# Kernel tuning notes

Measured on AMD Instinct MI355X. Metric: run time of the kernel, lower is better.

## Reference

```python
import jax, jax.numpy as jnp
import numpy as np

H, C = 16, 5           # GAT heads, per-head out channels
SIZE = 500             # max_pool_x size (time bins)
GAT_SLOPE, ACT_SLOPE = 0.2, 0.01


def _lrelu(x, s):
    return jnp.where(x >= 0, x, s * x)


def _gat(x, src, dst, ea, mask, W, We, a_s, a_d, a_e, b):
    # PyG GATConv: shared src/dst lin, edge_dim, self-loops already appended by caller
    N = x.shape[0]
    xp = (x @ W.T).reshape(N, H, C)                                   # [N,H,C]
    al = (jnp.einsum('nhc,hc->nh', xp, a_s)[src]
          + jnp.einsum('nhc,hc->nh', xp, a_d)[dst]
          + jnp.einsum('ehc,hc->eh', (ea @ We.T).reshape(-1, H, C), a_e))  # [E,H]
    al = _lrelu(al, GAT_SLOPE)
    if mask is not None:  # masked-out edges contribute nothing (equivalent to edge removal)
        al = jnp.where(mask[:, None], al, -jnp.inf)
    m = jax.ops.segment_max(al, dst, num_segments=N)                  # finite: every node has a self-loop
    e = jnp.exp(al - m[dst])
    coef = e / jax.ops.segment_sum(e, dst, num_segments=N)[dst]       # segment softmax over incoming edges
    out = jax.ops.segment_sum(coef[:, :, None] * xp[src], dst, num_segments=N)
    return out.reshape(N, H * C) + b


def _conv(x, w, b):
    y = jax.lax.conv_general_dilated(x, w, (2,), [(1, 1)],
                                     dimension_numbers=('NCH', 'OIH', 'NCH'))
    return y + b[None, :, None]


def _mlp(z, w1, b1, w2, b2, w3, b3):
    z = _lrelu(z @ w1.T + b1, ACT_SLOPE)
    z = _lrelu(z @ w2.T + b2, ACT_SLOPE)
    return z @ w3.T + b3


def _forward(x, edge_attr,
             gat1_W, gat1_We, gat1_as, gat1_ad, gat1_ae, gat1_b,
             gat2_W, gat2_We, gat2_as, gat2_ad, gat2_ae, gat2_b,
             conv1_w, conv1_b, conv2_w, conv2_b, conv3_w, conv3_b,
             chi_w1, chi_b1, chi_w2, chi_b2, chi_w3, chi_b3,
             rp_w1, rp_b1, rp_w2, rp_b2, rp_w3, rp_b3,
             t0_w1, t0_b1, t0_w2, t0_b2, t0_w3, t0_b3,
             edge_index, num_graphs):
    N = x.shape[0]
    loops = jnp.arange(N, dtype=edge_index.dtype)
    src = jnp.concatenate([edge_index[0], loops])
    dst = jnp.concatenate([edge_index[1], loops])
    ea = jnp.concatenate([edge_attr, jnp.zeros((N, edge_attr.shape[1]), edge_attr.dtype)], axis=0)
    timing = x[:, 2].astype(jnp.int32)   # non-differentiable, like .to(torch.long)

    h = _gat(x, src, dst, ea, None, gat1_W, gat1_We, gat1_as, gat1_ad, gat1_ae, gat1_b)
    mask2 = jnp.concatenate([edge_attr[:, 0] > 1.0, jnp.ones((N,), bool)])  # EdgeV[:,0]>1 + self loops
    h = _gat(h, src, dst, ea, mask2, gat2_W, gat2_We, gat2_as, gat2_ad, gat2_ae, gat2_b)

    # max_pool_x(cluster=Timing, batch, size=500): scatter-max into B*500 slots,
    # empty slots -> 0 (torch_scatter semantics); then view(-1, 80, 500)
    pooled = jax.ops.segment_max(h, timing, num_segments=num_graphs * SIZE)
    pooled = jnp.where(jnp.isfinite(pooled), pooled, 0.0)
    z = pooled.reshape(num_graphs, H * C, SIZE)

    z = _lrelu(_conv(z, conv1_w, conv1_b), ACT_SLOPE)   # [B,16,247]
    z = _lrelu(_conv(z, conv2_w, conv2_b), ACT_SLOPE)   # [B,16,120]
    z = _lrelu(_conv(z, conv3_w, conv3_b), ACT_SLOPE)   # [B,16,57]
    L = z.shape[-1]
    nw = (L - 10) // 10 + 1                              # MaxPool1d(k=10,s=10) -> 5
    z = z[..., :nw * 10].reshape(z.shape[0], z.shape[1], nw, 10).max(-1)
    z = z.reshape(z.shape[0], -1)                        # [B,80]

    chi0 = jnp.tanh(_mlp(z, chi_w1, chi_b1, chi_w2, chi_b2, chi_w3, chi_b3))
    rp = _mlp(z, rp_w1, rp_b1, rp_w2, rp_b2, rp_w3, rp_b3)
    t0 = _mlp(z, t0_w1, t0_b1, t0_w2, t0_b2, t0_w3, t0_b3)
    return jnp.concatenate([chi0, rp, t0], axis=1)       # [B,3]


def setup_inputs() -> dict:
    key = jax.random.key(0)
    ki = iter(jax.random.split(key, 50))
    N, E, B = 100_000, 1_200_000, 64
    x = jax.random.normal(next(ki), (N, 5), jnp.float32)
    timing = jax.random.randint(next(ki), (N,), 0, SIZE)
    x = x.at[:, 2].set(timing.astype(jnp.float32))       # Timing column holds integer bins
    src = jax.random.randint(next(ki), (E,), 0, N, dtype=jnp.int32)
    off = jax.random.randint(next(ki), (E,), 1, N, dtype=jnp.int32)
    dst = (src + off) % N                                # no pre-existing self-loops (PyG strips them)
    edge_index = jnp.stack([src, dst])
    edge_attr = jax.random.uniform(next(ki), (E, 2), jnp.float32) * 3.0  # ~2/3 pass col0>1 mask
    batch = jnp.sort(jax.random.randint(next(ki), (N,), 0, B, dtype=jnp.int32))

    def p(shape, scale=0.1):
        return jax.random.normal(next(ki), shape, jnp.float32) * scale

    return dict(
        x=x, edge_attr=edge_attr,
        gat1_W=p((80, 5)), gat1_We=p((80, 2)), gat1_as=p((16, 5)), gat1_ad=p((16, 5)), gat1_ae=p((16, 5)), gat1_b=p((80,)),
        gat2_W=p((80, 80)), gat2_We=p((80, 2)), gat2_as=p((16, 5)), gat2_ad=p((16, 5)), gat2_ae=p((16, 5)), gat2_b=p((80,)),
        conv1_w=p((16, 80, 10)), conv1_b=p((16,)),
        conv2_w=p((16, 16, 10)), conv2_b=p((16,)),
        conv3_w=p((16, 16, 10)), conv3_b=p((16,)),
        chi_w1=p((128, 80)), chi_b1=p((128,)), chi_w2=p((128, 128)), chi_b2=p((128,)), chi_w3=p((1, 128)), chi_b3=p((1,)),
        rp_w1=p((128, 80)), rp_b1=p((128,)), rp_w2=p((128, 128)), rp_b2=p((128,)), rp_w3=p((1, 128)), rp_b3=p((1,)),
        t0_w1=p((128, 80)), t0_b1=p((128,)), t0_w2=p((128, 128)), t0_b2=p((128,)), t0_w3=p((1, 128)), t0_b3=p((1,)),
        edge_index=edge_index, batch=batch, num_graphs=B)


def reference(x, edge_attr,
              gat1_W, gat1_We, gat1_as, gat1_ad, gat1_ae, gat1_b,
              gat2_W, gat2_We, gat2_as, gat2_ad, gat2_ae, gat2_b,
              conv1_w, conv1_b, conv2_w, conv2_b, conv3_w, conv3_b,
              chi_w1, chi_b1, chi_w2, chi_b2, chi_w3, chi_b3,
              rp_w1, rp_b1, rp_w2, rp_b2, rp_w3, rp_b3,
              t0_w1, t0_b1, t0_w2, t0_b2, t0_w3, t0_b3,
              edge_index, batch, num_graphs):
    del batch  # only used in torch to compute batch_size (passed here as num_graphs)
    return _forward(x, edge_attr,
                    gat1_W, gat1_We, gat1_as, gat1_ad, gat1_ae, gat1_b,
                    gat2_W, gat2_We, gat2_as, gat2_ad, gat2_ae, gat2_b,
                    conv1_w, conv1_b, conv2_w, conv2_b, conv3_w, conv3_b,
                    chi_w1, chi_b1, chi_w2, chi_b2, chi_w3, chi_b3,
                    rp_w1, rp_b1, rp_w2, rp_b2, rp_w3, rp_b3,
                    t0_w1, t0_b1, t0_w2, t0_b2, t0_w3, t0_b3,
                    edge_index, num_graphs)
```

## Files before the change

### kernel.cpp

```cpp
#include <hip/hip_runtime.h>
#include <math.h>

#define DEV static __device__ __forceinline__

DEV unsigned fenc(float f) {
    unsigned u = __float_as_uint(f);
    return (u & 0x80000000u) ? ~u : (u | 0x80000000u);
}
DEV float fdec(unsigned u) {
    return __uint_as_float((u & 0x80000000u) ? (u ^ 0x80000000u) : ~u);
}
DEV void atomic_max_u32(unsigned* p, unsigned v) {
    __hip_atomic_fetch_max(p, v, __ATOMIC_RELAXED, __HIP_MEMORY_SCOPE_AGENT);
}
DEV unsigned bf16(float f) {
    unsigned u = __float_as_uint(f);
    return (u + 0x7FFFu + ((u >> 16) & 1u)) >> 16;
}
DEV float unbf16(unsigned s) { return __uint_as_float(s << 16); }

__global__ void k_proj5t(const float* __restrict__ x, const float* __restrict__ W,
                         const float* __restrict__ a_s, const float* __restrict__ a_d,
                         unsigned short* __restrict__ xpb, float* __restrict__ dterm, int N) {
    int i = blockIdx.x * blockDim.x + threadIdx.x;
    if (i >= N * 16) return;
    int n = i >> 4, h = i & 15;
    float xr[5];
    #pragma unroll
    for (int j = 0; j < 5; ++j) xr[j] = x[(size_t)n * 5 + j];
    float o[5];
    #pragma unroll
    for (int c = 0; c < 5; ++c) {
        const float* wr = W + (size_t)(h * 5 + c) * 5;
        float s = 0.f;
        #pragma unroll
        for (int j = 0; j < 5; ++j) s += xr[j] * wr[j];
        o[c] = s;
    }
    float ss = 0.f, sd = 0.f;
    #pragma unroll
    for (int c = 0; c < 5; ++c) { ss += o[c] * a_s[h * 5 + c]; sd += o[c] * a_d[h * 5 + c]; }
    unsigned* p = (unsigned*)(xpb + (size_t)n * 96 + h * 6);
    p[0] = bf16(o[0]) | (bf16(o[1]) << 16);
    p[1] = bf16(o[2]) | (bf16(o[3]) << 16);
    p[2] = bf16(o[4]) | (bf16(ss) << 16);
    dterm[i] = sd;
}

__global__ __launch_bounds__(256) void k_proj80t(
    const unsigned short* __restrict__ in,
    const float* __restrict__ W,
    const float* __restrict__ a_s, const float* __restrict__ a_d,
    unsigned short* __restrict__ xpb, float* __restrict__ dterm, int N) {
    __shared__ float XS[16 * 136];
    __shared__ float WS[16 * 81];
    int tid = threadIdx.x;
    int n0 = blockIdx.x * 128;
    int h = tid & 15, ng = tid >> 4;

    float acc[8][5];
    #pragma unroll
    for (int j = 0; j < 8; ++j)
        #pragma unroll
        for (int c = 0; c < 5; ++c) acc[j][c] = 0.f;

    for (int k0 = 0; k0 < 80; k0 += 16) {
        __syncthreads();
        {
            int r = tid >> 1;
            int halfk = (tid & 1) * 8;
            int n = n0 + r; if (n >= N) n = N - 1;
            const uint4 v = *(const uint4*)(in + (size_t)n * 80 + k0 + halfk);
            unsigned uu[4] = {v.x, v.y, v.z, v.w};
            #pragma unroll
            for (int j = 0; j < 4; ++j) {
                XS[(halfk + 2 * j)     * 136 + r] = unbf16(uu[j] & 0xffff);
                XS[(halfk + 2 * j + 1) * 136 + r] = unbf16(uu[j] >> 16);
            }
        }
        {
            #pragma unroll
            for (int i = 0; i < 5; ++i) {
                int j = tid + i * 256;
                int oc = j >> 4, kk = j & 15;
                WS[kk * 81 + oc] = W[(size_t)oc * 80 + k0 + kk];
            }
        }
        __syncthreads();
        #pragma unroll
        for (int kk = 0; kk < 16; ++kk) {
            float4 xa = *(const float4*)&XS[kk * 136 + ng * 8];
            float4 xb = *(const float4*)&XS[kk * 136 + ng * 8 + 4];
            float wv[5];
            #pragma unroll
            for (int c = 0; c < 5; ++c) wv[c] = WS[kk * 81 + h * 5 + c];
            float xv[8] = {xa.x, xa.y, xa.z, xa.w, xb.x, xb.y, xb.z, xb.w};
            #pragma unroll
            for (int j = 0; j < 8; ++j)
                #pragma unroll
                for (int c = 0; c < 5; ++c) acc[j][c] += xv[j] * wv[c];
        }
    }
    float as_[5], ad_[5];
    #pragma unroll
    for (int c = 0; c < 5; ++c) { as_[c] = a_s[h * 5 + c]; ad_[c] = a_d[h * 5 + c]; }
    #pragma unroll
    for (int j = 0; j < 8; ++j) {
        int n = n0 + ng * 8 + j;
        if (n < N) {
            float ss = 0.f, sd = 0.f;
            #pragma unroll
            for (int c = 0; c < 5; ++c) { ss += acc[j][c] * as_[c]; sd += acc[j][c] * ad_[c]; }
            unsigned* p = (unsigned*)(xpb + (size_t)n * 96 + h * 6);
            p[0] = bf16(acc[j][0]) | (bf16(acc[j][1]) << 16);
            p[1] = bf16(acc[j][2]) | (bf16(acc[j][3]) << 16);
            p[2] = bf16(acc[j][4]) | (bf16(ss) << 16);
            dterm[n * 16 + h] = sd;
        }
    }
}

__global__ void k_hist(const int* __restrict__ dst, int* __restrict__ deg, int E) {
    int e4 = (blockIdx.x * blockDim.x + threadIdx.x) * 4;
    if (e4 >= E) return;
    if (e4 + 3 < E) {
        int4 d = *(const int4*)(dst + e4);
        __hip_atomic_fetch_add(&deg[d.x], 1, __ATOMIC_RELAXED, __HIP_MEMORY_SCOPE_AGENT);
        __hip_atomic_fetch_add(&deg[d.y], 1, __ATOMIC_RELAXED, __HIP_MEMORY_SCOPE_AGENT);
        __hip_atomic_fetch_add(&deg[d.z], 1, __ATOMIC_RELAXED, __HIP_MEMORY_SCOPE_AGENT);
        __hip_atomic_fetch_add(&deg[d.w], 1, __ATOMIC_RELAXED, __HIP_MEMORY_SCOPE_AGENT);
    } else {
        for (int e = e4; e < E; ++e)
            __hip_atomic_fetch_add(&deg[dst[e]], 1, __ATOMIC_RELAXED, __HIP_MEMORY_SCOPE_AGENT);
    }
}

#define SCAN_B 256
__global__ void k_bsum(const int* __restrict__ deg, int* __restrict__ bsum, int N) {
    __shared__ int sm[SCAN_B];
    int i = blockIdx.x * SCAN_B + threadIdx.x;
    sm[threadIdx.x] = (i < N) ? deg[i] : 0;
    __syncthreads();
    for (int s = SCAN_B / 2; s > 0; s >>= 1) {
        if (threadIdx.x < s) sm[threadIdx.x] += sm[threadIdx.x + s];
        __syncthreads();
    }
    if (threadIdx.x == 0) bsum[blockIdx.x] = sm[0];
}

__global__ void k_bscan(int* __restrict__ bsum, int G) {
    __shared__ int sm[512];
    int t = threadIdx.x;
    int orig = (t < G) ? bsum[t] : 0;
    sm[t] = orig;
    __syncthreads();
    for (int s = 1; s < 512; s <<= 1) {
        int v = (t >= s) ? sm[t - s] : 0;
        __syncthreads();
        sm[t] += v;
        __syncthreads();
    }
    if (t < G) bsum[t] = sm[t] - orig;
}

__global__ void k_apply(const int* __restrict__ deg, int* __restrict__ off,
                        int* __restrict__ bcur, const int* __restrict__ bsum, int N) {
    __shared__ int sm[SCAN_B];
    int i = blockIdx.x * SCAN_B + threadIdx.x;
    int v = (i < N) ? deg[i] : 0;
    sm[threadIdx.x] = v;
    __syncthreads();
    for (int s = 1; s < SCAN_B; s <<= 1) {
        int t = (threadIdx.x >= s) ? sm[threadIdx.x - s] : 0;
        __syncthreads();
        sm[threadIdx.x] += t;
        __syncthreads();
    }
    if (i < N) {
        int excl = bsum[blockIdx.x] + sm[threadIdx.x] - v;
        off[i] = excl;
        if ((i & 255) == 0) bcur[i >> 8] = excl;
        if (i == N - 1) off[N] = excl + v;
    }
}

#define BIN_TILE 4096
__global__ __launch_bounds__(256) void k_bin(const int* __restrict__ src,
        const int* __restrict__ dst, const float* __restrict__ ea,
        int* __restrict__ bcur, uint4* __restrict__ ebuf, int E, int NB) {
    __shared__ int cnt[512];
    __shared__ int base[512];
    int tid = threadIdx.x;
    for (int b = tid; b < NB; b += 256) cnt[b] = 0;
    __syncthreads();
    int e0 = blockIdx.x * BIN_TILE;
    #pragma unroll
    for (int k = 0; k < BIN_TILE / 256; ++k) {
        int e = e0 + k * 256 + tid;
        if (e < E) atomicAdd(&cnt[((unsigned)dst[e]) >> 8], 1);
    }
    __syncthreads();
    for (int b = tid; b < NB; b += 256) {
        int c = cnt[b];
        base[b] = c ? __hip_atomic_fetch_add(&bcur[b], c, __ATOMIC_RELAXED,
                                             __HIP_MEMORY_SCOPE_AGENT) : 0;
        cnt[b] = 0;
    }
    __syncthreads();
    #pragma unroll
    for (int k = 0; k < BIN_TILE / 256; ++k) {
        int e = e0 + k * 256 + tid;
        if (e < E) {
            int d = dst[e];
            int b = ((unsigned)d) >> 8;
            int r = atomicAdd(&cnt[b], 1);
            float a0 = ea[2 * e], a1 = ea[2 * e + 1];
            unsigned s = (unsigned)src[e] | (a0 > 1.0f ? 0x80000000u : 0u);
            ebuf[base[b] + r] = make_uint4(s, bf16(a0) | (bf16(a1) << 16), (unsigned)d, 0u);
        }
    }
}

__global__ __launch_bounds__(256) void k_perm(const int* __restrict__ off,
        const uint4* __restrict__ ebuf, uint2* __restrict__ erec, int N) {
    __shared__ int cur[256];
    int b = blockIdx.x, tid = threadIdx.x;
    int d0 = b << 8;
    int dEnd = d0 + 256; if (dEnd > N) dEnd = N;
    if (d0 + tid < N) cur[tid] = off[d0 + tid];
    int seg0 = off[d0], seg1 = off[dEnd];
    __syncthreads();
    for (int i = seg0 + tid; i < seg1; i += 256) {
        uint4 r = ebuf[i];
        int p = atomicAdd(&cur[(int)r.z - d0], 1);
        erec[p] = make_uint2(r.x, r.y);
    }
}

template<bool MASKED, bool OUT_BF16>
__global__ void k_gat(const int* __restrict__ off, const uint2* __restrict__ erec,
                      const float* __restrict__ dterm,
                      const float* __restrict__ We, const float* __restrict__ a_e,
                      const unsigned short* __restrict__ xpb,
                      const float* __restrict__ bias, void* __restrict__ hout, int N) {
    int i = blockIdx.x * blockDim.x + threadIdx.x;
    if (i >= N * 16) return;
    int d = i >> 4, h = i & 15;
    float q0 = 0.f, q1 = 0.f;
    #pragma unroll
    for (int c = 0; c < 5; ++c) {
        float ae = a_e[h * 5 + c];
        q0 += We[(h * 5 + c) * 2 + 0] * ae;
        q1 += We[(h * 5 + c) * 2 + 1] * ae;
    }
    float dt = dterm[i];
    int e0 = off[d], e1 = off[d + 1];

    float m, den = 1.f, n0, n1, n2, n3, n4;
    {
        const uint3 v = *(const uint3*)(xpb + (size_t)d * 96 + h * 6);
        n0 = unbf16(v.x & 0xffff); n1 = unbf16(v.x >> 16);
        n2 = unbf16(v.y & 0xffff); n3 = unbf16(v.y >> 16);
        n4 = unbf16(v.z & 0xffff);
        float sl = unbf16(v.z >> 16) + dt;
        m = fmaxf(sl, 0.2f * sl);
    }

    uint2 r_cur = make_uint2(0, 0), r_nxt = make_uint2(0, 0);
    uint3 v_cur = make_uint3(0, 0, 0), v_nxt = make_uint3(0, 0, 0);
    if (e0 < e1) {
        r_cur = erec[e0];
        if (!MASKED || (r_cur.x >> 31))
            v_cur = *(const uint3*)(xpb + (size_t)(r_cur.x & 0x7fffffff) * 96 + h * 6);
    }
    if (e0 + 1 < e1) r_nxt = erec[e0 + 1];
    for (int e = e0; e < e1; ++e) {
        uint2 r_n2 = make_uint2(0, 0);
        if (e + 2 < e1) r_n2 = erec[e + 2];
        if (e + 1 < e1 && (!MASKED || (r_nxt.x >> 31)))
            v_nxt = *(const uint3*)(xpb + (size_t)(r_nxt.x & 0x7fffffff) * 96 + h * 6);
        bool keep = !MASKED || (r_cur.x >> 31);
        if (keep) {
            float ea0 = unbf16(r_cur.y & 0xffff), ea1 = unbf16(r_cur.y >> 16);
            uint3 v = v_cur;
            float st = unbf16(v.z >> 16);
            float al = st + dt + ea0 * q0 + ea1 * q1;
            al = fmaxf(al, 0.2f * al);
            float x0 = unbf16(v.x & 0xffff), x1 = unbf16(v.x >> 16);
            float x2 = unbf16(v.y & 0xffff), x3 = unbf16(v.y >> 16);
            float x4 = unbf16(v.z & 0xffff);
            bool gt = al > m;
            float t = __expf(-fabsf(al - m));
            float c = gt ? t : 1.f;
            float w = gt ? 1.f : t;
            m = fmaxf(m, al);
            den = den * c + w;
            n0 = n0 * c + w * x0;
            n1 = n1 * c + w * x1;
            n2 = n2 * c + w * x2;
            n3 = n3 * c + w * x3;
            n4 = n4 * c + w * x4;
        }
        r_cur = r_nxt; r_nxt = r_n2; v_cur = v_nxt;
    }
    float inv = 1.0f / den;
    const float* br = bias + h * 5;
    float v0 = n0 * inv + br[0];
    float v1 = n1 * inv + br[1];
    float v2 = n2 * inv + br[2];
    float v3 = n3 * inv + br[3];
    float v4 = n4 * inv + br[4];
    if (OUT_BF16) {
        unsigned short* orow = (unsigned short*)hout + (size_t)d * 80 + h * 5;
        orow[0] = (unsigned short)bf16(v0);
        orow[1] = (unsigned short)bf16(v1);
        orow[2] = (unsigned short)bf16(v2);
        orow[3] = (unsigned short)bf16(v3);
        orow[4] = (unsigned short)bf16(v4);
    } else {
        float* orow = (float*)hout + (size_t)d * 80 + h * 5;
        orow[0] = v0; orow[1] = v1; orow[2] = v2; orow[3] = v3; orow[4] = v4;
    }
}

__global__ void k_pool8(const float* __restrict__ x, const float* __restrict__ h2,
                        unsigned* __restrict__ psl, int N) {
    int i = blockIdx.x * blockDim.x + threadIdx.x;
    if (i >= N * 80) return;
    int n = i / 80, ch = i % 80;
    int t = (int)x[(size_t)n * 5 + 2];
    unsigned* slice = psl + (size_t)(blockIdx.x & 7) * 40000;
    atomic_max_u32(&slice[t * 80 + ch], fenc(h2[i]));
}

__global__ void k_poolred(const unsigned* __restrict__ psl, float* __restrict__ pool) {
    int i = blockIdx.x * blockDim.x + threadIdx.x;
    if (i >= 40000) return;
    unsigned m = 0u;
    #pragma unroll
    for (int s = 0; s < 8; ++s) m = max(m, psl[s * 40000 + i]);
    pool[i] = (m == 0u) ? 0.f : fdec(m);
}

__global__ __launch_bounds__(256) void k_conv1(const float* __restrict__ pool,
        const float* __restrict__ w, const float* __restrict__ b,
        float* __restrict__ c1) {
    __shared__ float XS[80 * 140];
    __shared__ float WS[16 * 972];
    int gg = blockIdx.x >> 2, chunk = blockIdx.x & 3;
    int t0 = chunk * 62;
    int tid = threadIdx.x;
    for (int idx = tid; idx < 80 * 140; idx += 256) {
        int ic = idx / 140, j = idx % 140;
        int p = 2 * t0 - 1 + j;
        XS[idx] = (gg == 0 && p >= 0 && p < 500) ? pool[ic * 500 + p] : 0.f;
    }
    for (int idx = tid; idx < 12800; idx += 256) {
        int oc = idx / 800, r = idx % 800;
        int ic = r / 10, k = r % 10;
        WS[oc * 972 + ic * 12 + k] = w[idx];
    }
    __syncthreads();
    int oc = tid >> 4, tg = tid & 15;
    float acc0 = 0.f, acc1 = 0.f, acc2 = 0.f, acc3 = 0.f;
    for (int ic = 0; ic < 80; ++ic) {
        const float* xr = &XS[ic * 140 + 8 * tg];
        float4 xa = *(const float4*)xr;
        float4 xb = *(const float4*)(xr + 4);
        float4 xc = *(const float4*)(xr + 8);
        float4 xd = *(const float4*)(xr + 12);
        const float* wr = &WS[oc * 972 + ic * 12];
        float4 wa = *(const float4*)wr;
        float4 wb = *(const float4*)(wr + 4);
        float2 wc = *(const float2*)(wr + 8);
        float xv[16] = {xa.x, xa.y, xa.z, xa.w, xb.x, xb.y, xb.z, xb.w,
                        xc.x, xc.y, xc.z, xc.w, xd.x, xd.y, xd.z, xd.w};
        float wv[10] = {wa.x, wa.y, wa.z, wa.w, wb.x, wb.y, wb.z, wb.w, wc.x, wc.y};
        #pragma unroll
        for (int k = 0; k < 10; ++k) {
            acc0 += xv[k]     * wv[k];
            acc1 += xv[2 + k] * wv[k];
            acc2 += xv[4 + k] * wv[k];
            acc3 += xv[6 + k] * wv[k];
        }
    }
    float bb = b[oc];
    float accs[4] = {acc0, acc1, acc2, acc3};
    #pragma unroll
    for (int j = 0; j < 4; ++j) {
        int tt = 4 * tg + j;
        int t = t0 + tt;
        if (tt < 62 && t < 247) {
            float s = accs[j] + bb;
            c1[(size_t)gg * 3952 + oc * 247 + t] = s >= 0.f ? s : 0.01f * s;
        }
    }
}

__global__ __launch_bounds__(256) void k_convtail(
        const float* __restrict__ c1,
        const float* __restrict__ w2c, const float* __restrict__ b2c,
        const float* __restrict__ w3c, const float* __restrict__ b3c,
        float* __restrict__ zf) {
    __shared__ float Z1[16 * 248];
    __shared__ float Z2[16 * 121];
    __shared__ float Z3[16 * 58];
    int g = blockIdx.x, tid = threadIdx.x;
    for (int idx = tid; idx < 16 * 247; idx += 256) {
        int ic = idx / 247, t = idx % 247;
        Z1[ic * 248 + t] = c1[(size_t)g * 3952 + idx];
    }
    __syncthreads();
    for (int idx = tid; idx < 16 * 120; idx += 256) {
        int oc = idx / 120, t = idx % 120;
        float s = b2c[oc];
        for (int ic = 0; ic < 16; ++ic) {
            const float* xr = &Z1[ic * 248];
            const float* wr = &w2c[(oc * 16 + ic) * 10];
            #pragma unroll
            for (int k = 0; k < 10; ++k) {
                int p = 2 * t + k - 1;
                if (p >= 0 && p < 247) s += xr[p] * wr[k];
            }
        }
        Z2[oc * 121 + t] = s >= 0.f ? s : 0.01f * s;
    }
    __syncthreads();
    for (int idx = tid; idx < 16 * 57; idx += 256) {
        int oc = idx / 57, t = idx % 57;
        float s = b3c[oc];
        for (int ic = 0; ic < 16; ++ic) {
            const float* xr = &Z2[ic * 121];
            const float* wr = &w3c[(oc * 16 + ic) * 10];
            #pragma unroll
            for (int k = 0; k < 10; ++k) {
                int p = 2 * t + k - 1;
                if (p >= 0 && p < 120) s += xr[p] * wr[k];
            }
        }
        Z3[oc * 58 + t] = s >= 0.f ? s : 0.01f * s;
    }
    __syncthreads();
    if (tid < 80) {
        int ch = tid / 5, wd = tid % 5;
        const float* p = &Z3[ch * 58 + wd * 10];
        float m = p[0];
        #pragma unroll
        for (int k = 1; k < 10; ++k) m = fmaxf(m, p[k]);
        zf[g * 80 + tid] = m;
    }
}

struct HeadW { const float *w1, *b1, *w2, *b2, *w3, *b3; };

__global__ __launch_bounds__(128) void k_heads(const float* __restrict__ zf,
        HeadW hw0, HeadW hw1, HeadW hw2, float* __restrict__ houts) {
    __shared__ float ZF[80], HB[128], HC[128];
    __shared__ float partial[2];
    int g = blockIdx.x / 3, hd = blockIdx.x % 3;
    int tid = threadIdx.x;
    const HeadW hw = (hd == 0) ? hw0 : (hd == 1) ? hw1 : hw2;
    if (tid < 80) ZF[tid] = zf[g * 80 + tid];
    __syncthreads();
    float s = hw.b1[tid];
    for (int k = 0; k < 80; ++k) s += ZF[k] * hw.w1[tid * 80 + k];
    HB[tid] = s >= 0.f ? s : 0.01f * s;
    __syncthreads();
    s = hw.b2[tid];
    for (int k = 0; k < 128; ++k) s += HB[k] * hw.w2[tid * 128 + k];
    HC[tid] = s >= 0.f ? s : 0.01f * s;
    __syncthreads();
    float p = HC[tid] * hw.w3[tid];
    #pragma unroll
    for (int o = 32; o > 0; o >>= 1) p += __shfl_down(p, o, 64);
    if ((tid & 63) == 0) partial[tid >> 6] = p;
    __syncthreads();
    if (tid == 0) {
        float o = partial[0] + partial[1] + hw.b3[0];
        houts[g * 3 + hd] = (hd == 0) ? tanhf(o) : o;
    }
}

__global__ void k_bcast(const float* __restrict__ houts, float* __restrict__ out, int B3) {
    int i = blockIdx.x * blockDim.x + threadIdx.x;
    if (i >= B3) return;
    out[i] = (i < 3) ? houts[i] : houts[3 + (i % 3)];
}

extern "C" void kernel_launch(void* const* d_in, const int* in_sizes, int n_in,
                              void* d_out, int out_size, void* d_ws, size_t ws_size,
                              hipStream_t stream) {
    const float* x     = (const float*)d_in[0];
    const float* ea    = (const float*)d_in[1];
    const float* g1_W  = (const float*)d_in[2];
    const float* g1_We = (const float*)d_in[3];
    const float* g1_as = (const float*)d_in[4];
    const float* g1_ad = (const float*)d_in[5];
    const float* g1_ae = (const float*)d_in[6];
    const float* g1_b  = (const float*)d_in[7];
    const float* g2_W  = (const float*)d_in[8];
    const float* g2_We = (const float*)d_in[9];
    const float* g2_as = (const float*)d_in[10];
    const float* g2_ad = (const float*)d_in[11];
    const float* g2_ae = (const float*)d_in[12];
    const float* g2_b  = (const float*)d_in[13];
    const float* c1w = (const float*)d_in[14]; const float* c1b = (const float*)d_in[15];
    const float* c2w = (const float*)d_in[16]; const float* c2b = (const float*)d_in[17];
    const float* c3w = (const float*)d_in[18]; const float* c3b = (const float*)d_in[19];
    const int*   eidx = (const int*)d_in[38];
    float* out = (float*)d_out;

    const int N = in_sizes[0] / 5;
    const int E = in_sizes[38] / 2;
    const int B = out_size / 3;
    const int* src = eidx;
    const int* dst = eidx + E;

    float* ws = (float*)d_ws;
    size_t o = 0;
    auto alloc = [&](size_t n) { float* p = ws + o; o = (o + n + 3) & ~(size_t)3; return p; };
    unsigned short* xpb = (unsigned short*)alloc((size_t)N * 48);
    float*    Hbuf  = alloc((size_t)N * 80);
    float*    dterm = alloc((size_t)N * 16);
    int*      off   = (int*)alloc((size_t)N + 1);
    int*      cur   = (int*)alloc((size_t)N);
    int*      bsum  = (int*)alloc(512);
    int*      bcur  = (int*)alloc(512);
    uint4*    ebuf  = (uint4*)alloc((size_t)E * 4);
    uint2*    erec  = (uint2*)alloc((size_t)E * 2);
    unsigned* psl   = (unsigned*)alloc(8 * 40000);
    float*    pool  = alloc(40000);
    float*    c1    = alloc(2 * 3952);
    float*    zf    = alloc(2 * 80);
    float*    houts = alloc(8);

    const int BS = 256;
    auto blocks = [&](long long n) { return (int)((n + BS - 1) / BS); };
    const int G = (N + SCAN_B - 1) / SCAN_B;
    const int NB = (N + 255) / 256;

    hipMemsetAsync(cur, 0, (size_t)N * 4, stream);
    hipMemsetAsync(psl, 0, 8 * 40000 * 4, stream);
    k_hist<<<blocks((E + 3) / 4), BS, 0, stream>>>(dst, cur, E);
    k_bsum<<<G, SCAN_B, 0, stream>>>(cur, bsum, N);
    k_bscan<<<1, 512, 0, stream>>>(bsum, G);
    k_apply<<<G, SCAN_B, 0, stream>>>(cur, off, bcur, bsum, N);
    k_bin<<<(E + BIN_TILE - 1) / BIN_TILE, 256, 0, stream>>>(src, dst, ea, bcur, ebuf, E, NB);
    k_perm<<<NB, 256, 0, stream>>>(off, ebuf, erec, N);

    k_proj5t<<<blocks((long long)N * 16), BS, 0, stream>>>(x, g1_W, g1_as, g1_ad,
                                                           xpb, dterm, N);
    k_gat<false, true><<<blocks((long long)N * 16), BS, 0, stream>>>(
        off, erec, dterm, g1_We, g1_ae, xpb, g1_b, (void*)Hbuf, N);

    k_proj80t<<<(N + 127) / 128, 256, 0, stream>>>((const unsigned short*)Hbuf, g2_W,
                                                   g2_as, g2_ad, xpb, dterm, N);
    k_gat<true, false><<<blocks((long long)N * 16), BS, 0, stream>>>(
        off, erec, dterm, g2_We, g2_ae, xpb, g2_b, (void*)Hbuf, N);

    k_pool8<<<blocks((long long)N * 80), BS, 0, stream>>>(x, Hbuf, psl, N);
    k_poolred<<<blocks(40000), BS, 0, stream>>>(psl, pool);

    k_conv1<<<8, 256, 0, stream>>>(pool, c1w, c1b, c1);
    k_convtail<<<2, 256, 0, stream>>>(c1, c2w, c2b, c3w, c3b, zf);
    HeadW h0 = {(const float*)d_in[20], (const float*)d_in[21], (const float*)d_in[22],
                (const float*)d_in[23], (const float*)d_in[24], (const float*)d_in[25]};
    HeadW h1 = {(const float*)d_in[26], (const float*)d_in[27], (const float*)d_in[28],
                (const float*)d_in[29], (const float*)d_in[30], (const float*)d_in[31]};
    HeadW h2 = {(const float*)d_in[32], (const float*)d_in[33], (const float*)d_in[34],
                (const float*)d_in[35], (const float*)d_in[36], (const float*)d_in[37]};
    k_heads<<<6, 128, 0, stream>>>(zf, h0, h1, h2, houts);
    k_bcast<<<blocks(B * 3), BS, 0, stream>>>(houts, out, B * 3);
}
```

Baseline: 499.5 us.

## Split conv tail into per-channel kernels and widen conv1 grid

Measured after the change: 451.9 us. 1.11x faster.

```diff
diff --git a/kernel.cpp b/kernel.cpp
--- a/kernel.cpp
+++ b/kernel.cpp
@@ -345,15 +345,15 @@
 __global__ __launch_bounds__(256) void k_conv1(const float* __restrict__ pool,
         const float* __restrict__ w, const float* __restrict__ b,
         float* __restrict__ c1) {
-    __shared__ float XS[80 * 140];
+    __shared__ float XS[80 * 44];
     __shared__ float WS[16 * 972];
-    int gg = blockIdx.x >> 2, chunk = blockIdx.x & 3;
-    int t0 = chunk * 62;
+    int gg = blockIdx.x >> 4, chunk = blockIdx.x & 15;
+    int t0 = chunk * 16;
     int tid = threadIdx.x;
-    for (int idx = tid; idx < 80 * 140; idx += 256) {
-        int ic = idx / 140, j = idx % 140;
+    for (int idx = tid; idx < 80 * 44; idx += 256) {
+        int ic = idx / 44, j = idx % 44;
         int p = 2 * t0 - 1 + j;
-        XS[idx] = (gg == 0 && p >= 0 && p < 500) ? pool[ic * 500 + p] : 0.f;
+        XS[idx] = (gg == 0 && j < 41 && p >= 0 && p < 500) ? pool[ic * 500 + p] : 0.f;
     }
     for (int idx = tid; idx < 12800; idx += 256) {
         int oc = idx / 800, r = idx % 800;
@@ -362,105 +362,98 @@
     }
     __syncthreads();
     int oc = tid >> 4, tg = tid & 15;
-    float acc0 = 0.f, acc1 = 0.f, acc2 = 0.f, acc3 = 0.f;
+    float acc = 0.f;
     for (int ic = 0; ic < 80; ++ic) {
-        const float* xr = &XS[ic * 140 + 8 * tg];
-        float4 xa = *(const float4*)xr;
-        float4 xb = *(const float4*)(xr + 4);
-        float4 xc = *(const float4*)(xr + 8);
-        float4 xd = *(const float4*)(xr + 12);
+        const float* xr = &XS[ic * 44 + 2 * tg];
         const float* wr = &WS[oc * 972 + ic * 12];
-        float4 wa = *(const float4*)wr;
-        float4 wb = *(const float4*)(wr + 4);
-        float2 wc = *(const float2*)(wr + 8);
-        float xv[16] = {xa.x, xa.y, xa.z, xa.w, xb.x, xb.y, xb.z, xb.w,
-                        xc.x, xc.y, xc.z, xc.w, xd.x, xd.y, xd.z, xd.w};
-        float wv[10] = {wa.x, wa.y, wa.z, wa.w, wb.x, wb.y, wb.z, wb.w, wc.x, wc.y};
         #pragma unroll
-        for (int k = 0; k < 10; ++k) {
-            acc0 += xv[k]     * wv[k];
-            acc1 += xv[2 + k] * wv[k];
-            acc2 += xv[4 + k] * wv[k];
-            acc3 += xv[6 + k] * wv[k];
-        }
-    }
-    float bb = b[oc];
-    float accs[4] = {acc0, acc1, acc2, acc3};
-    #pragma unroll
-    for (int j = 0; j < 4; ++j) {
-        int tt = 4 * tg + j;
-        int t = t0 + tt;
-        if (tt < 62 && t < 247) {
-            float s = accs[j] + bb;
-            c1[(size_t)gg * 3952 + oc * 247 + t] = s >= 0.f ? s : 0.01f * s;
-        }
-    }
-}
-
-__global__ __launch_bounds__(256) void k_convtail(
-        const float* __restrict__ c1,
+        for (int k = 0; k < 10; ++k) acc += xr[k] * wr[k];
+    }
+    int t = t0 + tg;
+    if (t < 247) {
+        float s = acc + b[oc];
+        c1[(size_t)gg * 3952 + oc * 247 + t] = s >= 0.f ? s : 0.01f * s;
+    }
+}
+
+__global__ __launch_bounds__(128) void k_conv2(const float* __restrict__ c1,
         const float* __restrict__ w2c, const float* __restrict__ b2c,
-        const float* __restrict__ w3c, const float* __restrict__ b3c,
-        float* __restrict__ zf) {
+        float* __restrict__ c2g) {
     __shared__ float Z1[16 * 248];
-    __shared__ float Z2[16 * 121];
-    __shared__ float Z3[16 * 58];
-    int g = blockIdx.x, tid = threadIdx.x;
-    for (int idx = tid; idx < 16 * 247; idx += 256) {
+    __shared__ float WS[160];
+    int g = blockIdx.x >> 4, oc = blockIdx.x & 15;
+    int tid = threadIdx.x;
+    for (int idx = tid; idx < 16 * 247; idx += 128) {
         int ic = idx / 247, t = idx % 247;
         Z1[ic * 248 + t] = c1[(size_t)g * 3952 + idx];
     }
-    __syncthreads();
-    for (int idx = tid; idx < 16 * 120; idx += 256) {
-        int oc = idx / 120, t = idx % 120;
+    for (int idx = tid; idx < 160; idx += 128) WS[idx] = w2c[oc * 160 + idx];
+    __syncthreads();
+    if (tid < 120) {
         float s = b2c[oc];
+        #pragma unroll 4
         for (int ic = 0; ic < 16; ++ic) {
             const float* xr = &Z1[ic * 248];
-            const float* wr = &w2c[(oc * 16 + ic) * 10];
+            const float* wr = &WS[ic * 10];
             #pragma unroll
             for (int k = 0; k < 10; ++k) {
-                int p = 2 * t + k - 1;
+                int p = 2 * tid + k - 1;
                 if (p >= 0 && p < 247) s += xr[p] * wr[k];
             }
         }
-        Z2[oc * 121 + t] = s >= 0.f ? s : 0.01f * s;
-    }
-    __syncthreads();
-    for (int idx = tid; idx < 16 * 57; idx += 256) {
-        int oc = idx / 57, t = idx % 57;
+        c2g[g * 1920 + oc * 120 + tid] = s >= 0.f ? s : 0.01f * s;
+    }
+}
+
+__global__ __launch_bounds__(128) void k_conv3(const float* __restrict__ c2g,
+        const float* __restrict__ w3c, const float* __restrict__ b3c,
+        float* __restrict__ c3g) {
+    __shared__ float Z2[16 * 121];
+    __shared__ float WS[160];
+    int g = blockIdx.x >> 4, oc = blockIdx.x & 15;
+    int tid = threadIdx.x;
+    for (int idx = tid; idx < 16 * 120; idx += 128) {
+        int ic = idx / 120, t = idx % 120;
+        Z2[ic * 121 + t] = c2g[g * 1920 + idx];
+    }
+    for (int idx = tid; idx < 160; idx += 128) WS[idx] = w3c[oc * 160 + idx];
+    __syncthreads();
+    if (tid < 57) {
         float s = b3c[oc];
+        #pragma unroll 4
         for (int ic = 0; ic < 16; ++ic) {
             const float* xr = &Z2[ic * 121];
-            const float* wr = &w3c[(oc * 16 + ic) * 10];
+            const float* wr = &WS[ic * 10];
             #pragma unroll
             for (int k = 0; k < 10; ++k) {
-                int p = 2 * t + k - 1;
+                int p = 2 * tid + k - 1;
                 if (p >= 0 && p < 120) s += xr[p] * wr[k];
             }
         }
-        Z3[oc * 58 + t] = s >= 0.f ? s : 0.01f * s;
-    }
-    __syncthreads();
-    if (tid < 80) {
-        int ch = tid / 5, wd = tid % 5;
-        const float* p = &Z3[ch * 58 + wd * 10];
-        float m = p[0];
-        #pragma unroll
-        for (int k = 1; k < 10; ++k) m = fmaxf(m, p[k]);
-        zf[g * 80 + tid] = m;
+        c3g[g * 912 + oc * 57 + tid] = s >= 0.f ? s : 0.01f * s;
     }
 }
 
 struct HeadW { const float *w1, *b1, *w2, *b2, *w3, *b3; };
 
-__global__ __launch_bounds__(128) void k_heads(const float* __restrict__ zf,
+__global__ __launch_bounds__(128) void k_heads(const float* __restrict__ c3g,
         HeadW hw0, HeadW hw1, HeadW hw2, float* __restrict__ houts) {
+    __shared__ float Z3[16 * 57];
     __shared__ float ZF[80], HB[128], HC[128];
     __shared__ float partial[2];
     int g = blockIdx.x / 3, hd = blockIdx.x % 3;
     int tid = threadIdx.x;
     const HeadW hw = (hd == 0) ? hw0 : (hd == 1) ? hw1 : hw2;
-    if (tid < 80) ZF[tid] = zf[g * 80 + tid];
+    for (int idx = tid; idx < 912; idx += 128) Z3[idx] = c3g[g * 912 + idx];
+    __syncthreads();
+    if (tid < 80) {
+        int ch = tid / 5, wd = tid % 5;
+        const float* p = &Z3[ch * 57 + wd * 10];
+        float m = p[0];
+        #pragma unroll
+        for (int k = 1; k < 10; ++k) m = fmaxf(m, p[k]);
+        ZF[tid] = m;
+    }
     __syncthreads();
     float s = hw.b1[tid];
     for (int k = 0; k < 80; ++k) s += ZF[k] * hw.w1[tid * 80 + k];
@@ -531,7 +524,8 @@
     unsigned* psl   = (unsigned*)alloc(8 * 40000);
     float*    pool  = alloc(40000);
     float*    c1    = alloc(2 * 3952);
-    float*    zf    = alloc(2 * 80);
+    float*    c2g   = alloc(2 * 1920);
+    float*    c3g   = alloc(2 * 912);
     float*    houts = alloc(8);
 
     const int BS = 256;
@@ -561,14 +555,15 @@
     k_pool8<<<blocks((long long)N * 80), BS, 0, stream>>>(x, Hbuf, psl, N);
     k_poolred<<<blocks(40000), BS, 0, stream>>>(psl, pool);
 
-    k_conv1<<<8, 256, 0, stream>>>(pool, c1w, c1b, c1);
-    k_convtail<<<2, 256, 0, stream>>>(c1, c2w, c2b, c3w, c3b, zf);
+    k_conv1<<<32, 256, 0, stream>>>(pool, c1w, c1b, c1);
+    k_conv2<<<32, 128, 0, stream>>>(c1, c2w, c2b, c2g);
+    k_conv3<<<32, 128, 0, stream>>>(c2g, c3w, c3b, c3g);
     HeadW h0 = {(const float*)d_in[20], (const float*)d_in[21], (const float*)d_in[22],
                 (const float*)d_in[23], (const float*)d_in[24], (const float*)d_in[25]};
     HeadW h1 = {(const float*)d_in[26], (const float*)d_in[27], (const float*)d_in[28],
                 (const float*)d_in[29], (const float*)d_in[30], (const float*)d_in[31]};
     HeadW h2 = {(const float*)d_in[32], (const float*)d_in[33], (const float*)d_in[34],
                 (const float*)d_in[35], (const float*)d_in[36], (const float*)d_in[37]};
-    k_heads<<<6, 128, 0, stream>>>(zf, h0, h1, h2, houts);
+    k_heads<<<6, 128, 0, stream>>>(c3g, h0, h1, h2, houts);
     k_bcast<<<blocks(B * 3), BS, 0, stream>>>(houts, out, B * 3);
 }
```
